# Optimization experiments

Hardware: AMD Instinct MI355X
Metric: run time of the kernel (lower is better)

The kernel has to match this reference:

```python
import jax, jax.numpy as jnp
import numpy as np

S, B, H, R, V = 256, 64, 1024, 512, 512  # seq, batch, hidden, rep(vocab), output


def setup_inputs() -> dict:
    key = jax.random.key(0)
    k = jax.random.split(key, 11)
    n = lambda i, shape, s=0.05: jax.random.normal(k[i], shape, jnp.float32) * s
    return {
        "d_input": n(0, (S, B, R)),
        "cond": jax.random.randint(k[1], (B, 1), 0, 4),
        "e_input": jax.random.randint(k[2], (S, B), 0, R),
        "tf_flag": 1,
        "emb": n(3, (4, H)),
        "W_ih": n(4, (4 * H, R)),
        "W_hh": n(5, (4 * H, H)),
        "b_ih": n(6, (4 * H,)),
        "b_hh": n(7, (4 * H,)),
        "fc_w": n(8, (V, H)),
        "fc_b": n(9, (V,)),
    }


def _lstm_scan(xs, h0, c0, W_ih, W_hh, b_ih, b_hh):
    # xs: [S, B, R]; h0/c0: [B, H]. Torch gate order: i, f, g, o.
    Hd = h0.shape[-1]

    def cell(carry, x_t):
        h, c = carry
        gates = x_t @ W_ih.T + b_ih + h @ W_hh.T + b_hh  # [B, 4H]
        i, f, g, o = jnp.split(gates, 4, axis=-1)
        c = jax.nn.sigmoid(f) * c + jax.nn.sigmoid(i) * jnp.tanh(g)
        h = jax.nn.sigmoid(o) * jnp.tanh(c)
        return (h, c), h

    (h, c), outs = jax.lax.scan(cell, (h0, c0), xs)
    return outs, h, c


def reference(d_input, cond, e_input, tf_flag, emb, W_ih, W_hh, b_ih, b_hh, fc_w, fc_b):
    # cond_embedded = Embedding(cond.T) -> [1, B, H]; repeat over L*D=1 layers
    h0 = emb[cond[:, 0]]  # [B, H]
    c0 = h0
    if tf_flag:
        xs = jax.nn.one_hot(e_input, R, dtype=jnp.float32)  # [S, B, R]
    else:
        xs = d_input
    outs, h, c = _lstm_scan(xs, h0, c0, W_ih, W_hh, b_ih, b_hh)  # outs [S, B, H]
    logits = outs @ fc_w.T + fc_b  # [S, B, V]
    # CrossEntropyLoss(mean) over flattened tokens
    logp = jax.nn.log_softmax(logits.reshape(-1, V), axis=-1)
    labels = e_input.reshape(-1)
    loss = -jnp.mean(jnp.take_along_axis(logp, labels[:, None], axis=-1))
    return (logits, h[None], c[None], loss)
```

## Files before the change

kernel.cpp:

```cpp
#include <hip/hip_runtime.h>
#include <hip/hip_bf16.h>
#include <stdint.h>

#define S_LEN 256
#define BATCH 64
#define HID   1024
#define RDIM  512
#define VOC   512
#define GATES 4096

#define OFF_H    8388608u
#define OFF_C    8454144u
#define OFF_LOSS 8519680u

typedef __attribute__((ext_vector_type(8))) short short8;
typedef __attribute__((ext_vector_type(4))) float f32x4;
typedef __attribute__((ext_vector_type(4))) int   i32x4;
typedef unsigned long long u64;

#define HBUF_BYTES (128u * 1024u)
#define GT_S 65


__device__ inline unsigned short f2bf(float f) {
  unsigned u = __builtin_bit_cast(unsigned, f);
  return (unsigned short)((u + 0x7FFFu + ((u >> 16) & 1u)) >> 16);
}

__device__ inline u64 pack4(float a, float b, float c, float d) {
  return (u64)f2bf(a) | ((u64)f2bf(b) << 16) | ((u64)f2bf(c) << 32) | ((u64)f2bf(d) << 48);
}

__device__ inline f32x4 mfma16(short8 a, short8 b, f32x4 c) {
  return __builtin_amdgcn_mfma_f32_16x16x32_bf16(a, b, c, 0, 0, 0);
}

__device__ inline void stfrag8(char* p, u64 v) {
  __hip_atomic_store((u64*)p, v, __ATOMIC_RELAXED, __HIP_MEMORY_SCOPE_AGENT);
}

__device__ inline size_t fragoff(int b, int hcol) {
  int mt = b >> 4, kk = hcol >> 5;
  int lane = (b & 15) + (((hcol >> 3) & 3) << 4);
  return ((((size_t)mt * 32 + kk) * 64 + lane) << 4) + (size_t)((hcol & 7) * 2);
}

__device__ inline float sigm(float x) {
  return __builtin_amdgcn_rcpf(1.f + __expf(-x));
}
__device__ inline float tanh_(float x) {
  return 1.f - 2.f * __builtin_amdgcn_rcpf(__expf(2.f * x) + 1.f);
}

__global__ void __launch_bounds__(256) k_prep(
    const float* __restrict__ W_ih, const float* __restrict__ b_ih,
    const float* __restrict__ b_hh, const float* __restrict__ fc_w,
    float* __restrict__ T, unsigned short* __restrict__ fcw_bf,
    unsigned* __restrict__ flags, float* __restrict__ loss_slot)
{
  __shared__ float stage[64][65];
  const int bid = blockIdx.x, tid = threadIdx.x;
  if (bid < 512) {
    const int c0 = (bid >> 3) * 64, e0 = (bid & 7) * 64;
    for (int idx = tid; idx < 4096; idx += 256) {
      int i = idx >> 6, jj = idx & 63;
      stage[i][jj] = W_ih[(size_t)(c0 + i) * RDIM + e0 + jj];
    }
    __syncthreads();
    for (int idx = tid; idx < 4096; idx += 256) {
      int jj = idx >> 6, i = idx & 63;
      int c = c0 + i;
      T[(size_t)(e0 + jj) * GATES + c] = stage[i][jj] + b_ih[c] + b_hh[c];
    }
  } else if (bid < 516) {
    const size_t off = (size_t)(bid - 512) * 131072;
    for (int k = tid; k < 32768; k += 256) {
      float4 v = *(const float4*)(fc_w + off + (size_t)k * 4);
      ushort4 o;
      o.x = f2bf(v.x); o.y = f2bf(v.y); o.z = f2bf(v.z); o.w = f2bf(v.w);
      *(ushort4*)(fcw_bf + off + (size_t)k * 4) = o;
    }
  } else {
    for (int k = tid; k < 65536; k += 256)
      __hip_atomic_store(flags + k, 0u, __ATOMIC_RELAXED, __HIP_MEMORY_SCOPE_AGENT);
    if (tid == 0) loss_slot[0] = 0.f;
  }
}

__global__ void __launch_bounds__(256, 1) k_recur(
    const float* __restrict__ W_hh, const float* __restrict__ Tt,
    const int* __restrict__ e_input, const float* __restrict__ emb,
    const int* __restrict__ cond, const float* __restrict__ d_input,
    const int* __restrict__ tf_ptr, const float* __restrict__ W_ih,
    const float* __restrict__ b_ih, const float* __restrict__ b_hh,
    char* __restrict__ hbuf, unsigned* __restrict__ flags,
    unsigned short* __restrict__ outs_r, float* __restrict__ dout)
{
  extern __shared__ char smem[];
  char* Wlds = smem;
  float* gbufT = (float*)(smem + 131072);
  const int j = blockIdx.x;
  const int tid = threadIdx.x;
  const int w = tid >> 6, l = tid & 63;
  const int tf = tf_ptr[0];

  {
    const int nl = tid >> 2;
    const int kq = tid & 3;
    const int g = nl >> 4, hc = nl & 15;
    const float* wrow = W_hh + (size_t)(g * HID + j * 16 + hc) * HID + kq * 256;
    for (int k8 = 0; k8 < 32; ++k8) {
      const int k = kq * 256 + k8 * 8;
      float4 va = *(const float4*)(wrow + k8 * 8);
      float4 vb = *(const float4*)(wrow + k8 * 8 + 4);
      u64 lo = pack4(va.x, va.y, va.z, va.w);
      u64 hi = pack4(vb.x, vb.y, vb.z, vb.w);
      const int kk = k >> 5;
      const int lane = (nl & 15) + (((k >> 3) & 3) << 4);
      char* p = Wlds + (((size_t)(g * 32 + kk) * 64 + lane) << 4);
      *(u64*)p = lo;
      *(u64*)(p + 8) = hi;
    }
  }

  const int b = tid >> 2;
  const int hcl = (tid & 3) * 4;
  const int hcol = j * 16 + hcl;
  float cr[4];
  {
    const int cd = cond[b];
    float4 h0 = *(const float4*)(emb + (size_t)cd * HID + hcol);
    cr[0] = h0.x; cr[1] = h0.y; cr[2] = h0.z; cr[3] = h0.w;
    u64 pk = pack4(h0.x, h0.y, h0.z, h0.w);
    stfrag8(hbuf + fragoff(b, hcol), pk);
  }
  asm volatile("s_waitcnt vmcnt(0)" ::: "memory");
  __syncthreads();
  if (tid == 0)
    __hip_atomic_store(flags + j, 1u, __ATOMIC_RELAXED, __HIP_MEMORY_SCOPE_AGENT);

  for (int t = 0; t < S_LEN; ++t) {
    float4 t0, t1, t2, t3;
    if (tf != 0) {
      const float* Trow = Tt + (size_t)e_input[t * BATCH + b] * GATES;
      t0 = *(const float4*)(Trow + 0 * HID + hcol);
      t1 = *(const float4*)(Trow + 1 * HID + hcol);
      t2 = *(const float4*)(Trow + 2 * HID + hcol);
      t3 = *(const float4*)(Trow + 3 * HID + hcol);
    }

    if (tid < 64) {
      const unsigned* fp = flags + (size_t)t * 64 + tid;
      int guard = 0;
      while (__hip_atomic_load(fp, __ATOMIC_RELAXED, __HIP_MEMORY_SCOPE_AGENT) == 0u) {
        __builtin_amdgcn_s_sleep(1);
        if (++guard > (1 << 24)) break;
      }
    }
    __syncthreads();

    const char* hb = hbuf + (size_t)(t & 1) * HBUF_BYTES;
    const char* ap = hb + (((size_t)w * 32 * 64 + l) << 4);
    i32x4 a[32];
#pragma unroll
    for (int kk = 0; kk < 32; ++kk) {
      asm volatile("global_load_dwordx4 %0, %1, off sc0 sc1"
                   : "=v"(a[kk]) : "v"(ap + (size_t)kk * 1024));
    }
    asm volatile("s_waitcnt vmcnt(0)" ::: "memory");
    __builtin_amdgcn_sched_barrier(0);

    f32x4 acc[4];
    acc[0] = {0.f, 0.f, 0.f, 0.f}; acc[1] = {0.f, 0.f, 0.f, 0.f};
    acc[2] = {0.f, 0.f, 0.f, 0.f}; acc[3] = {0.f, 0.f, 0.f, 0.f};
#pragma unroll
    for (int kk = 0; kk < 32; ++kk) {
      const short8 A = __builtin_bit_cast(short8, a[kk]);
#pragma unroll
      for (int nt = 0; nt < 4; ++nt) {
        short8 B = *(const short8*)(Wlds + ((((size_t)nt * 32 + kk) * 64 + l) << 4));
        acc[nt] = mfma16(A, B, acc[nt]);
      }
    }
    {
      const int rb = (l >> 4) * 4, cb = l & 15;
#pragma unroll
      for (int nt = 0; nt < 4; ++nt)
#pragma unroll
        for (int r = 0; r < 4; ++r)
          gbufT[(nt * 16 + cb) * GT_S + w * 16 + rb + r] = acc[nt][r];
    }

    float gv[4][4];
#pragma unroll
    for (int g = 0; g < 4; ++g)
#pragma unroll
      for (int r = 0; r < 4; ++r)
        gv[g][r] = gbufT[(g * 16 + hcl + r) * GT_S + b];
    if (tf != 0) {
      gv[0][0] += t0.x; gv[0][1] += t0.y; gv[0][2] += t0.z; gv[0][3] += t0.w;
      gv[1][0] += t1.x; gv[1][1] += t1.y; gv[1][2] += t1.z; gv[1][3] += t1.w;
      gv[2][0] += t2.x; gv[2][1] += t2.y; gv[2][2] += t2.z; gv[2][3] += t2.w;
      gv[3][0] += t3.x; gv[3][1] += t3.y; gv[3][2] += t3.z; gv[3][3] += t3.w;
    } else {
      const float* x = d_input + ((size_t)t * BATCH + b) * RDIM;
#pragma unroll
      for (int g = 0; g < 4; ++g)
#pragma unroll
        for (int r = 0; r < 4; ++r) {
          const int row = g * HID + hcol + r;
          const float* wr = W_ih + (size_t)row * RDIM;
          float s = b_ih[row] + b_hh[row];
          for (int k = 0; k < RDIM; ++k) s += x[k] * wr[k];
          gv[g][r] += s;
        }
    }
    float hnew[4];
#pragma unroll
    for (int r = 0; r < 4; ++r) {
      float ig = sigm(gv[0][r]);
      float fg = sigm(gv[1][r]);
      float gg = tanh_(gv[2][r]);
      float og = sigm(gv[3][r]);
      cr[r] = fg * cr[r] + ig * gg;
      hnew[r] = og * tanh_(cr[r]);
    }
    const u64 pk = pack4(hnew[0], hnew[1], hnew[2], hnew[3]);
    *(u64*)(outs_r + (size_t)j * 262144 + ((size_t)t * BATCH + b) * 16 + hcl) = pk;
    stfrag8(hbuf + (size_t)((t + 1) & 1) * HBUF_BYTES + fragoff(b, hcol), pk);
    if (t == S_LEN - 1) {
      *(float4*)(dout + OFF_H + (size_t)b * HID + hcol) = make_float4(hnew[0], hnew[1], hnew[2], hnew[3]);
      *(float4*)(dout + OFF_C + (size_t)b * HID + hcol) = make_float4(cr[0], cr[1], cr[2], cr[3]);
    }
    asm volatile("s_waitcnt vmcnt(0)" ::: "memory");
    __syncthreads();
    if (tid == 0 && t < S_LEN - 1)
      __hip_atomic_store(flags + (size_t)(t + 1) * 64 + j, 1u,
                         __ATOMIC_RELAXED, __HIP_MEMORY_SCOPE_AGENT);
  }
}

__global__ void __launch_bounds__(256) k_gemm(
    const unsigned short* __restrict__ A,
    const unsigned short* __restrict__ Bw,
    const float* __restrict__ fcb, float* __restrict__ C)
{
  const int bid = blockIdx.x;
  const int m0 = (bid >> 3) * 64, n0 = (bid & 7) * 64;
  const int tid = threadIdx.x, w = tid >> 6, l = tid & 63;
  const int mt0 = (w >> 1) * 2, nt0 = (w & 1) * 2;
  f32x4 acc[2][2];
  acc[0][0] = {0.f, 0.f, 0.f, 0.f}; acc[0][1] = {0.f, 0.f, 0.f, 0.f};
  acc[1][0] = {0.f, 0.f, 0.f, 0.f}; acc[1][1] = {0.f, 0.f, 0.f, 0.f};
  const int ksel  = (l >> 4) & 3;
  const int jsel  = ksel >> 1;
  const int koffL = (ksel & 1) * 8;
  const int m_a0 = m0 + mt0 * 16 + (l & 15);
  const unsigned short* a0p = A + (size_t)jsel * 262144 + (size_t)m_a0 * 16 + koffL;
  const unsigned short* a1p = a0p + 16 * 16;
  const int koff = ksel * 8;
  const unsigned short* b0p = Bw + (size_t)(n0 + nt0 * 16 + (l & 15)) * HID + koff;
  const unsigned short* b1p = b0p + 16 * HID;
#pragma unroll 4
  for (int kk = 0; kk < 32; ++kk) {
    short8 A0 = *(const short8*)(a0p + (size_t)kk * 524288);
    short8 A1 = *(const short8*)(a1p + (size_t)kk * 524288);
    short8 B0 = *(const short8*)(b0p + kk * 32);
    short8 B1 = *(const short8*)(b1p + kk * 32);
    acc[0][0] = mfma16(A0, B0, acc[0][0]);
    acc[0][1] = mfma16(A0, B1, acc[0][1]);
    acc[1][0] = mfma16(A1, B0, acc[1][0]);
    acc[1][1] = mfma16(A1, B1, acc[1][1]);
  }
  const int rb = (l >> 4) * 4, cb = l & 15;
#pragma unroll
  for (int i2 = 0; i2 < 2; ++i2)
#pragma unroll
    for (int j2 = 0; j2 < 2; ++j2) {
      const int n = n0 + (nt0 + j2) * 16 + cb;
      const float fb = fcb[n];
#pragma unroll
      for (int r = 0; r < 4; ++r) {
        const int m = m0 + (mt0 + i2) * 16 + rb + r;
        C[(size_t)m * VOC + n] = acc[i2][j2][r] + fb;
      }
    }
}

__global__ void __launch_bounds__(256) k_loss(
    const float* __restrict__ logits, const int* __restrict__ labels,
    float* __restrict__ dout)
{
  const int tid = threadIdx.x, w = tid >> 6, l = tid & 63;
  float part = 0.f;
  for (int i = 0; i < 16; ++i) {
    const int row = blockIdx.x * 64 + w * 16 + i;
    const float* lr = logits + (size_t)row * VOC;
    float4 x0 = *(const float4*)(lr + l * 8);
    float4 x1 = *(const float4*)(lr + l * 8 + 4);
    float v[8] = {x0.x, x0.y, x0.z, x0.w, x1.x, x1.y, x1.z, x1.w};
    float mx = v[0];
#pragma unroll
    for (int k = 1; k < 8; ++k) mx = fmaxf(mx, v[k]);
    for (int off = 32; off; off >>= 1) mx = fmaxf(mx, __shfl_xor(mx, off));
    float se = 0.f;
#pragma unroll
    for (int k = 0; k < 8; ++k) se += __expf(v[k] - mx);
    for (int off = 32; off; off >>= 1) se += __shfl_xor(se, off);
    const float lse = mx + __logf(se);
    const int lab = labels[row];
    const int li = lab - l * 8;
    float pick = v[0];
#pragma unroll
    for (int k = 1; k < 8; ++k) pick = (li == k) ? v[k] : pick;
    float term = (li >= 0 && li < 8) ? (lse - pick) : 0.f;
    for (int off = 32; off; off >>= 1) term += __shfl_xor(term, off);
    part += term;
  }
  if (l == 0) atomicAdd(dout + OFF_LOSS, part * (1.f / 16384.f));
}

extern "C" void kernel_launch(void* const* d_in, const int* in_sizes, int n_in,
                              void* d_out, int out_size, void* d_ws, size_t ws_size,
                              hipStream_t stream) {
  const float* d_input = (const float*)d_in[0];
  const int*   cond    = (const int*)d_in[1];
  const int*   e_input = (const int*)d_in[2];
  const int*   tf_ptr  = (const int*)d_in[3];
  const float* emb     = (const float*)d_in[4];
  const float* W_ih    = (const float*)d_in[5];
  const float* W_hh    = (const float*)d_in[6];
  const float* b_ih    = (const float*)d_in[7];
  const float* b_hh    = (const float*)d_in[8];
  const float* fc_w    = (const float*)d_in[9];
  const float* fc_b    = (const float*)d_in[10];
  float* out = (float*)d_out;
  char*  ws  = (char*)d_ws;

  const size_t WS_T    = 0;
  const size_t WS_FCW  = 8388608;
  const size_t WS_OUTS = 9437184;
  const size_t WS_HBUF = 42991616;
  const size_t WS_FLAG = WS_HBUF + 2ull * HBUF_BYTES;
  char* hbuf = ws + WS_HBUF;
  unsigned* flags = (unsigned*)(ws + WS_FLAG);
  float* T = (float*)(ws + WS_T);
  unsigned short* fcw  = (unsigned short*)(ws + WS_FCW);
  unsigned short* outs = (unsigned short*)(ws + WS_OUTS);

  const int ldsz = 131072 + 64 * GT_S * 4;
  hipFuncSetAttribute((const void*)k_recur,
                      hipFuncAttributeMaxDynamicSharedMemorySize, ldsz);

  k_prep<<<dim3(517), dim3(256), 0, stream>>>(W_ih, b_ih, b_hh, fc_w, T, fcw,
                                              flags, out + OFF_LOSS);
  k_recur<<<dim3(64), dim3(256), ldsz, stream>>>(
      W_hh, T, e_input, emb, cond, d_input, tf_ptr, W_ih, b_ih, b_hh,
      hbuf, flags, outs, out);
  k_gemm<<<dim3(2048), dim3(256), 0, stream>>>(outs, fcw, fc_b, out);
  k_loss<<<dim3(256), dim3(256), 0, stream>>>(out, e_input, out);
}
```

Measured before the change: 1.528 ms.

## Keep W_hh slice in registers, split K across waves, per-wave byte flags

The recurrent kernel now holds each block's bf16 W_hh slice in registers, split by K across the four waves, instead of in LDS. Each wave computes partial gate sums over all batch tiles, reduced through a small static LDS buffer. The h-state loads are double-buffered against the MFMAs in four batch-tile chunks. The per-block ready flag becomes four per-wave bytes, so waves signal and poll independently without a block barrier before the store. This aims to cut LDS traffic and sync latency on the serial per-step critical path, at the cost of heavy register pressure and extra partial-sum reduction.

```diff
diff --git a/kernel.cpp b/kernel.cpp
--- a/kernel.cpp
+++ b/kernel.cpp
@@ -19,7 +19,6 @@
 typedef unsigned long long u64;
 
 #define HBUF_BYTES (128u * 1024u)
-#define GT_S 65
 
 
 __device__ inline unsigned short f2bf(float f) {
@@ -40,9 +39,9 @@
 }
 
 __device__ inline size_t fragoff(int b, int hcol) {
-  int mt = b >> 4, kk = hcol >> 5;
+  int bt = b >> 4, kk = hcol >> 5;
   int lane = (b & 15) + (((hcol >> 3) & 3) << 4);
-  return ((((size_t)mt * 32 + kk) * 64 + lane) << 4) + (size_t)((hcol & 7) * 2);
+  return ((((size_t)bt * 32 + kk) * 64 + lane) << 4) + (size_t)((hcol & 7) * 2);
 }
 
 __device__ inline float sigm(float x) {
@@ -96,48 +95,65 @@
     char* __restrict__ hbuf, unsigned* __restrict__ flags,
     unsigned short* __restrict__ outs_r, float* __restrict__ dout)
 {
-  extern __shared__ char smem[];
-  char* Wlds = smem;
-  float* gbufT = (float*)(smem + 131072);
+  __shared__ float pbuf[4][4][4][64][4];
   const int j = blockIdx.x;
   const int tid = threadIdx.x;
   const int w = tid >> 6, l = tid & 63;
   const int tf = tf_ptr[0];
 
-  {
-    const int nl = tid >> 2;
-    const int kq = tid & 3;
-    const int g = nl >> 4, hc = nl & 15;
-    const float* wrow = W_hh + (size_t)(g * HID + j * 16 + hc) * HID + kq * 256;
-    for (int k8 = 0; k8 < 32; ++k8) {
-      const int k = kq * 256 + k8 * 8;
-      float4 va = *(const float4*)(wrow + k8 * 8);
-      float4 vb = *(const float4*)(wrow + k8 * 8 + 4);
-      u64 lo = pack4(va.x, va.y, va.z, va.w);
-      u64 hi = pack4(vb.x, vb.y, vb.z, vb.w);
-      const int kk = k >> 5;
-      const int lane = (nl & 15) + (((k >> 3) & 3) << 4);
-      char* p = Wlds + (((size_t)(g * 32 + kk) * 64 + lane) << 4);
-      *(u64*)p = lo;
-      *(u64*)(p + 8) = hi;
-    }
-  }
-
-  const int b = tid >> 2;
-  const int hcl = (tid & 3) * 4;
+  short8 Breg[4][8];
+#pragma unroll
+  for (int nt = 0; nt < 4; ++nt) {
+#pragma unroll
+    for (int kkl = 0; kkl < 8; ++kkl) {
+      const float* wr = W_hh + (size_t)(nt * HID + j * 16 + (l & 15)) * HID
+                        + (w * 8 + kkl) * 32 + ((l >> 4) & 3) * 8;
+      float4 va = *(const float4*)wr;
+      float4 vb = *(const float4*)(wr + 4);
+      struct P { u64 a, b; } pr{pack4(va.x, va.y, va.z, va.w),
+                                pack4(vb.x, vb.y, vb.z, vb.w)};
+      Breg[nt][kkl] = __builtin_bit_cast(short8, pr);
+    }
+  }
+
+  const int b = w * 16 + (l & 15);
+  const int hcl = (l >> 4) * 4;
   const int hcol = j * 16 + hcl;
   float cr[4];
   {
     const int cd = cond[b];
     float4 h0 = *(const float4*)(emb + (size_t)cd * HID + hcol);
     cr[0] = h0.x; cr[1] = h0.y; cr[2] = h0.z; cr[3] = h0.w;
-    u64 pk = pack4(h0.x, h0.y, h0.z, h0.w);
-    stfrag8(hbuf + fragoff(b, hcol), pk);
+    stfrag8(hbuf + fragoff(b, hcol), pack4(h0.x, h0.y, h0.z, h0.w));
   }
   asm volatile("s_waitcnt vmcnt(0)" ::: "memory");
-  __syncthreads();
-  if (tid == 0)
-    __hip_atomic_store(flags + j, 1u, __ATOMIC_RELAXED, __HIP_MEMORY_SCOPE_AGENT);
+  if (l == 0)
+    __hip_atomic_store((unsigned char*)(flags + j) + w, (unsigned char)1,
+                       __ATOMIC_RELAXED, __HIP_MEMORY_SCOPE_AGENT);
+
+#define ISSUE(buf, bt)                                                        \
+  _Pragma("unroll")                                                           \
+  for (int kkl = 0; kkl < 8; ++kkl)                                           \
+    asm volatile("global_load_dwordx4 %0, %1, off sc0 sc1"                    \
+                 : "=v"(buf[kkl])                                             \
+                 : "v"(hbl + (bt) * 32768 + kkl * 1024));
+
+#define MFMA_BT(bt, buf)                                                      \
+  _Pragma("unroll")                                                           \
+  for (int nt = 0; nt < 4; ++nt)                                              \
+    acc[nt] = mfma16(Breg[nt][0], __builtin_bit_cast(short8, buf[0]),         \
+                     (f32x4){0.f, 0.f, 0.f, 0.f});                            \
+  _Pragma("unroll")                                                           \
+  for (int kkl = 1; kkl < 8; ++kkl)                                           \
+    _Pragma("unroll")                                                         \
+    for (int nt = 0; nt < 4; ++nt)                                            \
+      acc[nt] = mfma16(Breg[nt][kkl], __builtin_bit_cast(short8, buf[kkl]),   \
+                       acc[nt]);
+
+#define WRITE_BT(bt)                                                          \
+  _Pragma("unroll")                                                           \
+  for (int nt = 0; nt < 4; ++nt)                                              \
+    *(f32x4*)&pbuf[w][bt][nt][l][0] = acc[nt];
 
   for (int t = 0; t < S_LEN; ++t) {
     float4 t0, t1, t2, t3;
@@ -147,61 +163,63 @@
       t1 = *(const float4*)(Trow + 1 * HID + hcol);
       t2 = *(const float4*)(Trow + 2 * HID + hcol);
       t3 = *(const float4*)(Trow + 3 * HID + hcol);
-    }
-
-    if (tid < 64) {
-      const unsigned* fp = flags + (size_t)t * 64 + tid;
+      __builtin_amdgcn_sched_barrier(0);
+    }
+
+    {
+      const unsigned* fp = flags + (size_t)t * 64 + l;
       int guard = 0;
-      while (__hip_atomic_load(fp, __ATOMIC_RELAXED, __HIP_MEMORY_SCOPE_AGENT) == 0u) {
+      while (__hip_atomic_load(fp, __ATOMIC_RELAXED, __HIP_MEMORY_SCOPE_AGENT)
+             != 0x01010101u) {
         __builtin_amdgcn_s_sleep(1);
         if (++guard > (1 << 24)) break;
       }
     }
+    asm volatile("s_waitcnt vmcnt(0)" ::: "memory");
+    __builtin_amdgcn_sched_barrier(0);
+
+    const char* hbl = hbuf + (size_t)(t & 1) * HBUF_BYTES
+                      + (size_t)w * 8192 + (size_t)l * 16;
+    i32x4 cbA[8], cbB[8];
+    f32x4 acc[4];
+    ISSUE(cbA, 0)
+    ISSUE(cbB, 1)
+    asm volatile("s_waitcnt vmcnt(8)" ::: "memory");
+    __builtin_amdgcn_sched_barrier(0);
+    MFMA_BT(0, cbA)
+    ISSUE(cbA, 2)
+    WRITE_BT(0)
+    asm volatile("s_waitcnt vmcnt(8)" ::: "memory");
+    __builtin_amdgcn_sched_barrier(0);
+    MFMA_BT(1, cbB)
+    ISSUE(cbB, 3)
+    WRITE_BT(1)
+    asm volatile("s_waitcnt vmcnt(8)" ::: "memory");
+    __builtin_amdgcn_sched_barrier(0);
+    MFMA_BT(2, cbA)
+    WRITE_BT(2)
+    asm volatile("s_waitcnt vmcnt(0)" ::: "memory");
+    __builtin_amdgcn_sched_barrier(0);
+    MFMA_BT(3, cbB)
+    WRITE_BT(3)
     __syncthreads();
 
-    const char* hb = hbuf + (size_t)(t & 1) * HBUF_BYTES;
-    const char* ap = hb + (((size_t)w * 32 * 64 + l) << 4);
-    i32x4 a[32];
-#pragma unroll
-    for (int kk = 0; kk < 32; ++kk) {
-      asm volatile("global_load_dwordx4 %0, %1, off sc0 sc1"
-                   : "=v"(a[kk]) : "v"(ap + (size_t)kk * 1024));
-    }
-    asm volatile("s_waitcnt vmcnt(0)" ::: "memory");
-    __builtin_amdgcn_sched_barrier(0);
-
-    f32x4 acc[4];
-    acc[0] = {0.f, 0.f, 0.f, 0.f}; acc[1] = {0.f, 0.f, 0.f, 0.f};
-    acc[2] = {0.f, 0.f, 0.f, 0.f}; acc[3] = {0.f, 0.f, 0.f, 0.f};
-#pragma unroll
-    for (int kk = 0; kk < 32; ++kk) {
-      const short8 A = __builtin_bit_cast(short8, a[kk]);
-#pragma unroll
-      for (int nt = 0; nt < 4; ++nt) {
-        short8 B = *(const short8*)(Wlds + ((((size_t)nt * 32 + kk) * 64 + l) << 4));
-        acc[nt] = mfma16(A, B, acc[nt]);
+    f32x4 gq[4];
+#pragma unroll
+    for (int g = 0; g < 4; ++g) {
+      f32x4 s = *(const f32x4*)&pbuf[0][w][g][l][0];
+#pragma unroll
+      for (int kh = 1; kh < 4; ++kh) {
+        f32x4 p = *(const f32x4*)&pbuf[kh][w][g][l][0];
+        s[0] += p[0]; s[1] += p[1]; s[2] += p[2]; s[3] += p[3];
       }
-    }
-    {
-      const int rb = (l >> 4) * 4, cb = l & 15;
-#pragma unroll
-      for (int nt = 0; nt < 4; ++nt)
-#pragma unroll
-        for (int r = 0; r < 4; ++r)
-          gbufT[(nt * 16 + cb) * GT_S + w * 16 + rb + r] = acc[nt][r];
-    }
-
-    float gv[4][4];
-#pragma unroll
-    for (int g = 0; g < 4; ++g)
-#pragma unroll
-      for (int r = 0; r < 4; ++r)
-        gv[g][r] = gbufT[(g * 16 + hcl + r) * GT_S + b];
+      gq[g] = s;
+    }
     if (tf != 0) {
-      gv[0][0] += t0.x; gv[0][1] += t0.y; gv[0][2] += t0.z; gv[0][3] += t0.w;
-      gv[1][0] += t1.x; gv[1][1] += t1.y; gv[1][2] += t1.z; gv[1][3] += t1.w;
-      gv[2][0] += t2.x; gv[2][1] += t2.y; gv[2][2] += t2.z; gv[2][3] += t2.w;
-      gv[3][0] += t3.x; gv[3][1] += t3.y; gv[3][2] += t3.z; gv[3][3] += t3.w;
+      gq[0][0] += t0.x; gq[0][1] += t0.y; gq[0][2] += t0.z; gq[0][3] += t0.w;
+      gq[1][0] += t1.x; gq[1][1] += t1.y; gq[1][2] += t1.z; gq[1][3] += t1.w;
+      gq[2][0] += t2.x; gq[2][1] += t2.y; gq[2][2] += t2.z; gq[2][3] += t2.w;
+      gq[3][0] += t3.x; gq[3][1] += t3.y; gq[3][2] += t3.z; gq[3][3] += t3.w;
     } else {
       const float* x = d_input + ((size_t)t * BATCH + b) * RDIM;
 #pragma unroll
@@ -212,16 +230,16 @@
           const float* wr = W_ih + (size_t)row * RDIM;
           float s = b_ih[row] + b_hh[row];
           for (int k = 0; k < RDIM; ++k) s += x[k] * wr[k];
-          gv[g][r] += s;
+          gq[g][r] += s;
         }
     }
     float hnew[4];
 #pragma unroll
     for (int r = 0; r < 4; ++r) {
-      float ig = sigm(gv[0][r]);
-      float fg = sigm(gv[1][r]);
-      float gg = tanh_(gv[2][r]);
-      float og = sigm(gv[3][r]);
+      float ig = sigm(gq[0][r]);
+      float fg = sigm(gq[1][r]);
+      float gg = tanh_(gq[2][r]);
+      float og = sigm(gq[3][r]);
       cr[r] = fg * cr[r] + ig * gg;
       hnew[r] = og * tanh_(cr[r]);
     }
@@ -233,11 +251,14 @@
       *(float4*)(dout + OFF_C + (size_t)b * HID + hcol) = make_float4(cr[0], cr[1], cr[2], cr[3]);
     }
     asm volatile("s_waitcnt vmcnt(0)" ::: "memory");
-    __syncthreads();
-    if (tid == 0 && t < S_LEN - 1)
-      __hip_atomic_store(flags + (size_t)(t + 1) * 64 + j, 1u,
+    if (l == 0 && t < S_LEN - 1)
+      __hip_atomic_store((unsigned char*)(flags + (size_t)(t + 1) * 64 + j) + w,
+                         (unsigned char)1,
                          __ATOMIC_RELAXED, __HIP_MEMORY_SCOPE_AGENT);
   }
+#undef ISSUE
+#undef MFMA_BT
+#undef WRITE_BT
 }
 
 __global__ void __launch_bounds__(256) k_gemm(
@@ -348,13 +369,9 @@
   unsigned short* fcw  = (unsigned short*)(ws + WS_FCW);
   unsigned short* outs = (unsigned short*)(ws + WS_OUTS);
 
-  const int ldsz = 131072 + 64 * GT_S * 4;
-  hipFuncSetAttribute((const void*)k_recur,
-                      hipFuncAttributeMaxDynamicSharedMemorySize, ldsz);
-
   k_prep<<<dim3(517), dim3(256), 0, stream>>>(W_ih, b_ih, b_hh, fc_w, T, fcw,
                                               flags, out + OFF_LOSS);
-  k_recur<<<dim3(64), dim3(256), ldsz, stream>>>(
+  k_recur<<<dim3(64), dim3(256), 0, stream>>>(
       W_hh, T, e_input, emb, cond, d_input, tf_ptr, W_ih, b_ih, b_hh,
       hbuf, flags, outs, out);
   k_gemm<<<dim3(2048), dim3(256), 0, stream>>>(outs, fcw, fc_b, out);
```

Result: slower. 1.839 ms (+20.3%).

## Swap MFMA operands to drop LDS transpose and pipeline h loads with MFMA

Applied to the files above, without the earlier changes.

The recurrent kernel now feeds W_hh as the A operand and h as the B operand, so each lane's accumulator directly holds the four gate values for its own batch row and hidden columns. This removes the LDS staging buffer, its transposed write and read, and the extra LDS allocation. The thread-to-(batch, column) mapping is changed to match the MFMA output layout. The single full wait on the 32 global h loads is split into four partial waits, so MFMAs on early K chunks can start while later loads are still in flight. Together these aim to shorten each serial timestep of the recurrence.

```diff
diff --git a/kernel.cpp b/kernel.cpp
--- a/kernel.cpp
+++ b/kernel.cpp
@@ -19,7 +19,6 @@
 typedef unsigned long long u64;
 
 #define HBUF_BYTES (128u * 1024u)
-#define GT_S 65
 
 
 __device__ inline unsigned short f2bf(float f) {
@@ -40,9 +39,9 @@
 }
 
 __device__ inline size_t fragoff(int b, int hcol) {
-  int mt = b >> 4, kk = hcol >> 5;
+  int bt = b >> 4, kk = hcol >> 5;
   int lane = (b & 15) + (((hcol >> 3) & 3) << 4);
-  return ((((size_t)mt * 32 + kk) * 64 + lane) << 4) + (size_t)((hcol & 7) * 2);
+  return ((((size_t)bt * 32 + kk) * 64 + lane) << 4) + (size_t)((hcol & 7) * 2);
 }
 
 __device__ inline float sigm(float x) {
@@ -98,7 +97,6 @@
 {
   extern __shared__ char smem[];
   char* Wlds = smem;
-  float* gbufT = (float*)(smem + 131072);
   const int j = blockIdx.x;
   const int tid = threadIdx.x;
   const int w = tid >> 6, l = tid & 63;
@@ -123,21 +121,31 @@
     }
   }
 
-  const int b = tid >> 2;
-  const int hcl = (tid & 3) * 4;
+  const int b = w * 16 + (l & 15);
+  const int hcl = (l >> 4) * 4;
   const int hcol = j * 16 + hcl;
   float cr[4];
   {
     const int cd = cond[b];
     float4 h0 = *(const float4*)(emb + (size_t)cd * HID + hcol);
     cr[0] = h0.x; cr[1] = h0.y; cr[2] = h0.z; cr[3] = h0.w;
-    u64 pk = pack4(h0.x, h0.y, h0.z, h0.w);
-    stfrag8(hbuf + fragoff(b, hcol), pk);
+    stfrag8(hbuf + fragoff(b, hcol), pack4(h0.x, h0.y, h0.z, h0.w));
   }
   asm volatile("s_waitcnt vmcnt(0)" ::: "memory");
   __syncthreads();
   if (tid == 0)
     __hip_atomic_store(flags + j, 1u, __ATOMIC_RELAXED, __HIP_MEMORY_SCOPE_AGENT);
+
+#define MFMA_BT(bt)                                                           \
+  _Pragma("unroll")                                                           \
+  for (int kkl = 0; kkl < 8; ++kkl) {                                         \
+    const int kk = (bt) * 8 + kkl;                                            \
+    _Pragma("unroll")                                                         \
+    for (int nt = 0; nt < 4; ++nt) {                                          \
+      short8 Wv = *(const short8*)(Wlds + ((((size_t)nt * 32 + kk) * 64 + l) << 4)); \
+      acc[nt] = mfma16(Wv, __builtin_bit_cast(short8, a[kk]), acc[nt]);       \
+    }                                                                         \
+  }
 
   for (int t = 0; t < S_LEN; ++t) {
     float4 t0, t1, t2, t3;
@@ -159,49 +167,41 @@
     }
     __syncthreads();
 
-    const char* hb = hbuf + (size_t)(t & 1) * HBUF_BYTES;
-    const char* ap = hb + (((size_t)w * 32 * 64 + l) << 4);
+    const char* hbl = hbuf + (size_t)(t & 1) * HBUF_BYTES
+                      + (((size_t)w * 32 * 64 + l) << 4);
     i32x4 a[32];
 #pragma unroll
     for (int kk = 0; kk < 32; ++kk) {
       asm volatile("global_load_dwordx4 %0, %1, off sc0 sc1"
-                   : "=v"(a[kk]) : "v"(ap + (size_t)kk * 1024));
-    }
-    asm volatile("s_waitcnt vmcnt(0)" ::: "memory");
-    __builtin_amdgcn_sched_barrier(0);
-
+                   : "=v"(a[kk]) : "v"(hbl + (size_t)kk * 1024));
+    }
     f32x4 acc[4];
     acc[0] = {0.f, 0.f, 0.f, 0.f}; acc[1] = {0.f, 0.f, 0.f, 0.f};
     acc[2] = {0.f, 0.f, 0.f, 0.f}; acc[3] = {0.f, 0.f, 0.f, 0.f};
-#pragma unroll
-    for (int kk = 0; kk < 32; ++kk) {
-      const short8 A = __builtin_bit_cast(short8, a[kk]);
-#pragma unroll
-      for (int nt = 0; nt < 4; ++nt) {
-        short8 B = *(const short8*)(Wlds + ((((size_t)nt * 32 + kk) * 64 + l) << 4));
-        acc[nt] = mfma16(A, B, acc[nt]);
-      }
-    }
-    {
-      const int rb = (l >> 4) * 4, cb = l & 15;
-#pragma unroll
-      for (int nt = 0; nt < 4; ++nt)
-#pragma unroll
-        for (int r = 0; r < 4; ++r)
-          gbufT[(nt * 16 + cb) * GT_S + w * 16 + rb + r] = acc[nt][r];
-    }
-
-    float gv[4][4];
+    asm volatile("s_waitcnt vmcnt(24)" ::: "memory");
+    __builtin_amdgcn_sched_barrier(0);
+    MFMA_BT(0)
+    asm volatile("s_waitcnt vmcnt(16)" ::: "memory");
+    __builtin_amdgcn_sched_barrier(0);
+    MFMA_BT(1)
+    asm volatile("s_waitcnt vmcnt(8)" ::: "memory");
+    __builtin_amdgcn_sched_barrier(0);
+    MFMA_BT(2)
+    asm volatile("s_waitcnt vmcnt(0)" ::: "memory");
+    __builtin_amdgcn_sched_barrier(0);
+    MFMA_BT(3)
+
+    float gq[4][4];
 #pragma unroll
     for (int g = 0; g < 4; ++g)
 #pragma unroll
       for (int r = 0; r < 4; ++r)
-        gv[g][r] = gbufT[(g * 16 + hcl + r) * GT_S + b];
+        gq[g][r] = acc[g][r];
     if (tf != 0) {
-      gv[0][0] += t0.x; gv[0][1] += t0.y; gv[0][2] += t0.z; gv[0][3] += t0.w;
-      gv[1][0] += t1.x; gv[1][1] += t1.y; gv[1][2] += t1.z; gv[1][3] += t1.w;
-      gv[2][0] += t2.x; gv[2][1] += t2.y; gv[2][2] += t2.z; gv[2][3] += t2.w;
-      gv[3][0] += t3.x; gv[3][1] += t3.y; gv[3][2] += t3.z; gv[3][3] += t3.w;
+      gq[0][0] += t0.x; gq[0][1] += t0.y; gq[0][2] += t0.z; gq[0][3] += t0.w;
+      gq[1][0] += t1.x; gq[1][1] += t1.y; gq[1][2] += t1.z; gq[1][3] += t1.w;
+      gq[2][0] += t2.x; gq[2][1] += t2.y; gq[2][2] += t2.z; gq[2][3] += t2.w;
+      gq[3][0] += t3.x; gq[3][1] += t3.y; gq[3][2] += t3.z; gq[3][3] += t3.w;
     } else {
       const float* x = d_input + ((size_t)t * BATCH + b) * RDIM;
 #pragma unroll
@@ -212,22 +212,22 @@
           const float* wr = W_ih + (size_t)row * RDIM;
           float s = b_ih[row] + b_hh[row];
           for (int k = 0; k < RDIM; ++k) s += x[k] * wr[k];
-          gv[g][r] += s;
+          gq[g][r] += s;
         }
     }
     float hnew[4];
 #pragma unroll
     for (int r = 0; r < 4; ++r) {
-      float ig = sigm(gv[0][r]);
-      float fg = sigm(gv[1][r]);
-      float gg = tanh_(gv[2][r]);
-      float og = sigm(gv[3][r]);
+      float ig = sigm(gq[0][r]);
+      float fg = sigm(gq[1][r]);
+      float gg = tanh_(gq[2][r]);
+      float og = sigm(gq[3][r]);
       cr[r] = fg * cr[r] + ig * gg;
       hnew[r] = og * tanh_(cr[r]);
     }
     const u64 pk = pack4(hnew[0], hnew[1], hnew[2], hnew[3]);
+    stfrag8(hbuf + (size_t)((t + 1) & 1) * HBUF_BYTES + fragoff(b, hcol), pk);
     *(u64*)(outs_r + (size_t)j * 262144 + ((size_t)t * BATCH + b) * 16 + hcl) = pk;
-    stfrag8(hbuf + (size_t)((t + 1) & 1) * HBUF_BYTES + fragoff(b, hcol), pk);
     if (t == S_LEN - 1) {
       *(float4*)(dout + OFF_H + (size_t)b * HID + hcol) = make_float4(hnew[0], hnew[1], hnew[2], hnew[3]);
       *(float4*)(dout + OFF_C + (size_t)b * HID + hcol) = make_float4(cr[0], cr[1], cr[2], cr[3]);
@@ -238,6 +238,7 @@
       __hip_atomic_store(flags + (size_t)(t + 1) * 64 + j, 1u,
                          __ATOMIC_RELAXED, __HIP_MEMORY_SCOPE_AGENT);
   }
+#undef MFMA_BT
 }
 
 __global__ void __launch_bounds__(256) k_gemm(
@@ -348,13 +349,12 @@
   unsigned short* fcw  = (unsigned short*)(ws + WS_FCW);
   unsigned short* outs = (unsigned short*)(ws + WS_OUTS);
 
-  const int ldsz = 131072 + 64 * GT_S * 4;
   hipFuncSetAttribute((const void*)k_recur,
-                      hipFuncAttributeMaxDynamicSharedMemorySize, ldsz);
+                      hipFuncAttributeMaxDynamicSharedMemorySize, 131072);
 
   k_prep<<<dim3(517), dim3(256), 0, stream>>>(W_ih, b_ih, b_hh, fc_w, T, fcw,
                                               flags, out + OFF_LOSS);
-  k_recur<<<dim3(64), dim3(256), ldsz, stream>>>(
+  k_recur<<<dim3(64), dim3(256), 131072, stream>>>(
       W_hh, T, e_input, emb, cond, d_input, tf_ptr, W_ih, b_ih, b_hh,
       hbuf, flags, outs, out);
   k_gemm<<<dim3(2048), dim3(256), 0, stream>>>(outs, fcw, fc_b, out);
```

After: 1.429 ms (median of 2 runs). 6.5% less time.
